# Optimization experiments

Measured on AMD Instinct MI355X. Metric: run time of the kernel, lower is better.

The kernel has to match this reference:

```python
import jax, jax.numpy as jnp
import numpy as np

TAU = 0.5
EPS = 1e-12  # torch F.normalize default eps


def setup_inputs() -> dict:
    key = jax.random.key(0)
    ks = jax.random.split(key, 6)
    N, D = 8192, 512
    return {
        "pri_embedding": jax.random.normal(ks[0], (N, D), dtype=jnp.float32),
        "aux_embedding": jax.random.normal(ks[1], (N, D), dtype=jnp.float32),
        "W1": jax.random.normal(ks[2], (D, D), dtype=jnp.float32) * (1.0 / np.sqrt(D)),
        "b1": jax.random.normal(ks[3], (D,), dtype=jnp.float32) * 0.01,
        "W2": jax.random.normal(ks[4], (D, D), dtype=jnp.float32) * (1.0 / np.sqrt(D)),
        "b2": jax.random.normal(ks[5], (D,), dtype=jnp.float32) * 0.01,
    }


def _projection(z, W1, b1, W2, b2):
    h = jax.nn.elu(z @ W1.T + b1)
    return h @ W2.T + b2


def _normalize(z):
    norm = jnp.sqrt(jnp.sum(z * z, axis=-1, keepdims=True))
    return z / jnp.maximum(norm, EPS)


def _semi_loss(z1, z2):
    n1 = _normalize(z1)
    n2 = _normalize(z2)
    refl = jnp.exp((n1 @ n1.T) / TAU)      # [N, N]
    between = jnp.exp((n1 @ n2.T) / TAU)   # [N, N]
    num = jnp.diagonal(between)
    den = refl.sum(axis=1) + between.sum(axis=1) - jnp.diagonal(refl)
    return -jnp.log(num / den)


def reference(pri_embedding, aux_embedding, W1, b1, W2, b2):
    h1 = _projection(pri_embedding, W1, b1, W2, b2)
    h2 = _projection(aux_embedding, W1, b1, W2, b2)
    l1 = _semi_loss(h1, h2)
    l2 = _semi_loss(h2, h1)
    ret = (l1 + l2) * 0.5
    return ret.mean()
```

## Files before the change

kernel.cpp:

```cpp
#include <hip/hip_runtime.h>
#include <stdint.h>

typedef unsigned short u16;
typedef __bf16 bf16x8 __attribute__((ext_vector_type(8)));
typedef float f32x4 __attribute__((ext_vector_type(4)));

#define NROWS 8192
#define DDIM 512

#define GLOAD_LDS16(g, l)                                            \
  __builtin_amdgcn_global_load_lds(                                  \
      (const __attribute__((address_space(1))) void*)(g),            \
      (__attribute__((address_space(3))) void*)(l), 16, 0, 0)

__device__ __forceinline__ u16 f32_to_bf16(float f) {
  union { float f; unsigned u; } v; v.f = f;
  unsigned r = v.u + 0x7fffu + ((v.u >> 16) & 1u);
  return (u16)(r >> 16);
}

#define GEMM_CORE(A_, B_)                                                     \
  const int t = threadIdx.x;                                                  \
  const int lane = t & 63;                                                    \
  const int w = t >> 6;                                                       \
  const int wr = w >> 1, wc = w & 1;                                          \
  const int r0 = t >> 2, c0 = (t & 3) * 8;                                    \
  const u16* ApA = A_ + (size_t)(tileM + r0) * 512 + c0;                      \
  const u16* ApB = ApA + (size_t)64 * 512;                                    \
  const u16* BpA = B_ + (size_t)(tileN + r0) * 512 + c0;                      \
  const u16* BpB = BpA + (size_t)64 * 512;                                    \
  f32x4 acc[4][4] = {};                                                       \
  const int lrow = lane & 15;                                                 \
  const int kb = (lane >> 4) * 8;                                             \
  for (int k0 = 0; k0 < 512; k0 += 64) {                                      \
    __syncthreads();                                                          \
    GLOAD_LDS16(ApA + k0,      &As[t * 8]);                                   \
    GLOAD_LDS16(ApB + k0,      &As[(t + 256) * 8]);                           \
    GLOAD_LDS16(ApA + k0 + 32, &As[(t + 512) * 8]);                           \
    GLOAD_LDS16(ApB + k0 + 32, &As[(t + 768) * 8]);                           \
    GLOAD_LDS16(BpA + k0,      &Bs[t * 8]);                                   \
    GLOAD_LDS16(BpB + k0,      &Bs[(t + 256) * 8]);                           \
    GLOAD_LDS16(BpA + k0 + 32, &Bs[(t + 512) * 8]);                           \
    GLOAD_LDS16(BpB + k0 + 32, &Bs[(t + 768) * 8]);                           \
    __syncthreads();                                                          \
    _Pragma("unroll")                                                         \
    for (int s = 0; s < 2; s++) {                                             \
      bf16x8 af[4], bfr[4];                                                   \
      _Pragma("unroll")                                                       \
      for (int m = 0; m < 4; m++)                                             \
        af[m] = *(const bf16x8*)&As[s * 4096 + (wr * 64 + m * 16 + lrow) * 32 + kb]; \
      _Pragma("unroll")                                                       \
      for (int n = 0; n < 4; n++)                                             \
        bfr[n] = *(const bf16x8*)&Bs[s * 4096 + (wc * 64 + n * 16 + lrow) * 32 + kb]; \
      _Pragma("unroll")                                                       \
      for (int m = 0; m < 4; m++)                                             \
        _Pragma("unroll")                                                     \
        for (int n = 0; n < 4; n++)                                           \
          acc[m][n] = __builtin_amdgcn_mfma_f32_16x16x32_bf16(af[m], bfr[n], acc[m][n], 0, 0, 0); \
    }                                                                         \
  }                                                                           \
  const int rowg = (lane >> 4) * 4;                                           \
  const int col = lane & 15;

__global__ void cast2_f32_bf16(const float* __restrict__ a, u16* __restrict__ oa, int n4a,
                               const float* __restrict__ b, u16* __restrict__ ob, int n4b) {
  int i = blockIdx.x * blockDim.x + threadIdx.x;
  const float* src; u16* dst;
  if (i < n4a) { src = a; dst = oa; }
  else if (i < n4a + n4b) { i -= n4a; src = b; dst = ob; }
  else return;
  float4 v = reinterpret_cast<const float4*>(src)[i];
  ushort4 o;
  o.x = f32_to_bf16(v.x); o.y = f32_to_bf16(v.y);
  o.z = f32_to_bf16(v.z); o.w = f32_to_bf16(v.w);
  reinterpret_cast<ushort4*>(dst)[i] = o;
}

template <int EPI>
__global__ void __launch_bounds__(256)
gemm_proj(const u16* __restrict__ Ag, const u16* __restrict__ Bg,
          const float* __restrict__ bias,
          u16* __restrict__ outB, float* __restrict__ outF)
{
  __shared__ __align__(16) u16 As[2 * 128 * 32];
  __shared__ __align__(16) u16 Bs[2 * 128 * 32];
  const int tileM = blockIdx.y * 128;
  const int tileN = blockIdx.x * 128;

  GEMM_CORE(Ag, Bg)

#pragma unroll
  for (int m = 0; m < 4; m++) {
    int grow = tileM + wr * 64 + m * 16 + rowg;
#pragma unroll
    for (int n = 0; n < 4; n++) {
      int gcol = tileN + wc * 64 + n * 16 + col;
      float bv = bias[gcol];
#pragma unroll
      for (int r = 0; r < 4; r++) {
        float v = acc[m][n][r] + bv;
        if (EPI == 0) {
          v = v > 0.0f ? v : (__expf(v) - 1.0f);
          outB[(size_t)(grow + r) * 512 + gcol] = f32_to_bf16(v);
        } else {
          outF[(size_t)(grow + r) * 512 + gcol] = v;
        }
      }
    }
  }
}

__global__ void __launch_bounds__(256)
sim_merged(const u16* __restrict__ n1, const u16* __restrict__ n2,
           float* __restrict__ rs11, float* __restrict__ rs12,
           float* __restrict__ cs12, float* __restrict__ rs22)
{
  __shared__ __align__(16) u16 As[2 * 128 * 32];
  __shared__ __align__(16) u16 Bs[2 * 128 * 32];

  int bid = blockIdx.x;
  const u16 *A, *B; float *rsum, *csum; bool sym; int by, bx;
  if (bid < 4096) {
    by = bid >> 6; bx = bid & 63;
    A = n1; B = n2; rsum = rs12; csum = cs12; sym = false;
  } else {
    int tau = bid - 4096;
    if (tau >= 2080) { tau -= 2080; A = n2; rsum = rs22; }
    else             {              A = n1; rsum = rs11; }
    B = A; csum = rsum; sym = true;
    by = (int)(64.5f - sqrtf(64.5f * 64.5f - 2.0f * (float)tau));
    if (by < 0) by = 0;
    while (64 * (by + 1) - ((by + 1) * by) / 2 <= tau) by++;
    while (64 * by - (by * (by - 1)) / 2 > tau) by--;
    bx = by + (tau - (64 * by - (by * (by - 1)) / 2));
  }
  const int tileM = by * 128, tileN = bx * 128;

  GEMM_CORE(A, B)

#pragma unroll
  for (int m = 0; m < 4; m++) {
#pragma unroll
    for (int r = 0; r < 4; r++) {
      float s = 0.0f;
#pragma unroll
      for (int n = 0; n < 4; n++) {
        float e = __expf(acc[m][n][r] * 2.0f);
        acc[m][n][r] = e;
        s += e;
      }
      s += __shfl_xor(s, 1);
      s += __shfl_xor(s, 2);
      s += __shfl_xor(s, 4);
      s += __shfl_xor(s, 8);
      if (col == 0)
        atomicAdd(&rsum[tileM + wr * 64 + m * 16 + rowg + r], s);
    }
  }
  if (!sym || tileM != tileN) {
    float* cdst = sym ? rsum : csum;
#pragma unroll
    for (int n = 0; n < 4; n++) {
      float s = 0.0f;
#pragma unroll
      for (int m = 0; m < 4; m++)
#pragma unroll
        for (int r = 0; r < 4; r++) s += acc[m][n][r];
      s += __shfl_xor(s, 16);
      s += __shfl_xor(s, 32);
      if ((lane >> 4) == 0)
        atomicAdd(&cdst[tileN + wc * 64 + n * 16 + col], s);
    }
  }
}

__global__ void __launch_bounds__(256)
normalize_rows(const float* __restrict__ p1, const float* __restrict__ p2,
               u16* __restrict__ n1, u16* __restrict__ n2, float* __restrict__ d12)
{
  int row = blockIdx.x;
  int t = threadIdx.x;
  const float* r1 = p1 + (size_t)row * 512;
  const float* r2 = p2 + (size_t)row * 512;
  float a0 = r1[t], a1 = r1[t + 256];
  float b0 = r2[t], b1 = r2[t + 256];
  float ss1 = a0 * a0 + a1 * a1;
  float ss2 = b0 * b0 + b1 * b1;
  float dt  = a0 * b0 + a1 * b1;
#pragma unroll
  for (int m = 1; m < 64; m <<= 1) {
    ss1 += __shfl_xor(ss1, m);
    ss2 += __shfl_xor(ss2, m);
    dt  += __shfl_xor(dt, m);
  }
  __shared__ float sh[3][4];
  int w = t >> 6;
  if ((t & 63) == 0) { sh[0][w] = ss1; sh[1][w] = ss2; sh[2][w] = dt; }
  __syncthreads();
  ss1 = sh[0][0] + sh[0][1] + sh[0][2] + sh[0][3];
  ss2 = sh[1][0] + sh[1][1] + sh[1][2] + sh[1][3];
  dt  = sh[2][0] + sh[2][1] + sh[2][2] + sh[2][3];
  float i1 = 1.0f / fmaxf(sqrtf(ss1), 1e-12f);
  float i2 = 1.0f / fmaxf(sqrtf(ss2), 1e-12f);
  n1[(size_t)row * 512 + t]       = f32_to_bf16(a0 * i1);
  n1[(size_t)row * 512 + t + 256] = f32_to_bf16(a1 * i1);
  n2[(size_t)row * 512 + t]       = f32_to_bf16(b0 * i2);
  n2[(size_t)row * 512 + t + 256] = f32_to_bf16(b1 * i2);
  if (t == 0) d12[row] = dt * i1 * i2;
}

__global__ void __launch_bounds__(256)
loss_reduce(const float* __restrict__ rs11, const float* __restrict__ rs12,
            const float* __restrict__ cs12, const float* __restrict__ rs22,
            const float* __restrict__ d12, float* __restrict__ out)
{
  int t = threadIdx.x;
  const float e2 = __expf(2.0f);
  float s = 0.0f;
  for (int i = t; i < NROWS; i += 256) {
    float den1 = rs11[i] + rs12[i] - e2;
    float den2 = rs22[i] + cs12[i] - e2;
    s += 0.5f * (logf(den1) + logf(den2)) - 2.0f * d12[i];
  }
#pragma unroll
  for (int m = 1; m < 64; m <<= 1) s += __shfl_xor(s, m);
  __shared__ float sh[4];
  if ((t & 63) == 0) sh[t >> 6] = s;
  __syncthreads();
  if (t == 0) out[0] = (sh[0] + sh[1] + sh[2] + sh[3]) * (1.0f / (float)NROWS);
}

extern "C" void kernel_launch(void* const* d_in, const int* in_sizes, int n_in,
                              void* d_out, int out_size, void* d_ws, size_t ws_size,
                              hipStream_t stream) {
  (void)in_sizes; (void)n_in; (void)out_size; (void)ws_size;
  const float* pri = (const float*)d_in[0];
  const float* aux = (const float*)d_in[1];
  const float* W1  = (const float*)d_in[2];
  const float* b1  = (const float*)d_in[3];
  const float* W2  = (const float*)d_in[4];
  const float* b2  = (const float*)d_in[5];
  float* out = (float*)d_out;

  const int N = NROWS, D = DDIM;
  char* ws = (char*)d_ws;
  size_t off = 0;
  auto alloc = [&](size_t bytes) -> void* {
    void* p = ws + off;
    off += (bytes + 255) & ~(size_t)255;
    return p;
  };
  u16* prib = (u16*)alloc((size_t)N * D * 2);
  u16* auxb = (u16*)alloc((size_t)N * D * 2);
  u16* W1b  = (u16*)alloc((size_t)D * D * 2);
  u16* W2b  = (u16*)alloc((size_t)D * D * 2);
  u16* h1b  = (u16*)alloc((size_t)N * D * 2);
  u16* h2b  = (u16*)alloc((size_t)N * D * 2);
  float* p1 = (float*)alloc((size_t)N * D * 4);
  float* p2 = (float*)alloc((size_t)N * D * 4);
  u16* n1b  = (u16*)alloc((size_t)N * D * 2);
  u16* n2b  = (u16*)alloc((size_t)N * D * 2);
  float* d12  = (float*)alloc((size_t)N * 4);
  float* rs11 = (float*)alloc((size_t)N * 4);
  float* rs12 = (float*)alloc((size_t)N * 4);
  float* cs12 = (float*)alloc((size_t)N * 4);
  float* rs22 = (float*)alloc((size_t)N * 4);
  (void)auxb; (void)h2b; (void)p2;

  hipMemsetAsync(rs11, 0, (size_t)4 * N * 4, stream);

  const int n4e = N * D / 4, n4w = D * D / 4;
  cast2_f32_bf16<<<(n4e + n4w + 255) / 256, 256, 0, stream>>>(pri, prib, n4e, W1, W1b, n4w);
  cast2_f32_bf16<<<(n4e + n4w + 255) / 256, 256, 0, stream>>>(aux, auxb, n4e, W2, W2b, n4w);

  dim3 gproj(D / 128, 2 * N / 128);
  gemm_proj<0><<<gproj, 256, 0, stream>>>(prib, W1b, b1, h1b, nullptr);
  gemm_proj<1><<<gproj, 256, 0, stream>>>(h1b, W2b, b2, nullptr, p1);

  normalize_rows<<<N, 256, 0, stream>>>(p1, p2, n1b, n2b, d12);

  sim_merged<<<4096 + 2 * 2080, 256, 0, stream>>>(n1b, n2b, rs11, rs12, cs12, rs22);

  loss_reduce<<<1, 256, 0, stream>>>(rs11, rs12, cs12, rs22, d12, out);
}
```

Before: 413.7 us.

## Enlarge similarity GEMM tiles to 256x256 with double-buffered LDS prefetch

The fused similarity/exp/row-sum kernel moves from 128x128 tiles with 256 threads to 256x256 tiles with 512 threads (8 waves, 128x64 per wave). The K loop now stages the next K-slice into a second LDS buffer while computing on the current one, so there is one barrier per step instead of two. Block indices are remapped so that consecutive launch IDs spread across groups of 260. The GEMM core macro is inlined into the projection kernel. The goal is more operand reuse per global/LDS load and fewer exposed memory stalls, at the cost of 128KB of LDS per block, which limits occupancy and coarsens work on the symmetric triangle.

```diff
diff --git a/kernel.cpp b/kernel.cpp
--- a/kernel.cpp
+++ b/kernel.cpp
@@ -18,49 +18,6 @@
   unsigned r = v.u + 0x7fffu + ((v.u >> 16) & 1u);
   return (u16)(r >> 16);
 }
-
-#define GEMM_CORE(A_, B_)                                                     \
-  const int t = threadIdx.x;                                                  \
-  const int lane = t & 63;                                                    \
-  const int w = t >> 6;                                                       \
-  const int wr = w >> 1, wc = w & 1;                                          \
-  const int r0 = t >> 2, c0 = (t & 3) * 8;                                    \
-  const u16* ApA = A_ + (size_t)(tileM + r0) * 512 + c0;                      \
-  const u16* ApB = ApA + (size_t)64 * 512;                                    \
-  const u16* BpA = B_ + (size_t)(tileN + r0) * 512 + c0;                      \
-  const u16* BpB = BpA + (size_t)64 * 512;                                    \
-  f32x4 acc[4][4] = {};                                                       \
-  const int lrow = lane & 15;                                                 \
-  const int kb = (lane >> 4) * 8;                                             \
-  for (int k0 = 0; k0 < 512; k0 += 64) {                                      \
-    __syncthreads();                                                          \
-    GLOAD_LDS16(ApA + k0,      &As[t * 8]);                                   \
-    GLOAD_LDS16(ApB + k0,      &As[(t + 256) * 8]);                           \
-    GLOAD_LDS16(ApA + k0 + 32, &As[(t + 512) * 8]);                           \
-    GLOAD_LDS16(ApB + k0 + 32, &As[(t + 768) * 8]);                           \
-    GLOAD_LDS16(BpA + k0,      &Bs[t * 8]);                                   \
-    GLOAD_LDS16(BpB + k0,      &Bs[(t + 256) * 8]);                           \
-    GLOAD_LDS16(BpA + k0 + 32, &Bs[(t + 512) * 8]);                           \
-    GLOAD_LDS16(BpB + k0 + 32, &Bs[(t + 768) * 8]);                           \
-    __syncthreads();                                                          \
-    _Pragma("unroll")                                                         \
-    for (int s = 0; s < 2; s++) {                                             \
-      bf16x8 af[4], bfr[4];                                                   \
-      _Pragma("unroll")                                                       \
-      for (int m = 0; m < 4; m++)                                             \
-        af[m] = *(const bf16x8*)&As[s * 4096 + (wr * 64 + m * 16 + lrow) * 32 + kb]; \
-      _Pragma("unroll")                                                       \
-      for (int n = 0; n < 4; n++)                                             \
-        bfr[n] = *(const bf16x8*)&Bs[s * 4096 + (wc * 64 + n * 16 + lrow) * 32 + kb]; \
-      _Pragma("unroll")                                                       \
-      for (int m = 0; m < 4; m++)                                             \
-        _Pragma("unroll")                                                     \
-        for (int n = 0; n < 4; n++)                                           \
-          acc[m][n] = __builtin_amdgcn_mfma_f32_16x16x32_bf16(af[m], bfr[n], acc[m][n], 0, 0, 0); \
-    }                                                                         \
-  }                                                                           \
-  const int rowg = (lane >> 4) * 4;                                           \
-  const int col = lane & 15;
 
 __global__ void cast2_f32_bf16(const float* __restrict__ a, u16* __restrict__ oa, int n4a,
                                const float* __restrict__ b, u16* __restrict__ ob, int n4b) {
@@ -87,8 +44,47 @@
   const int tileM = blockIdx.y * 128;
   const int tileN = blockIdx.x * 128;
 
-  GEMM_CORE(Ag, Bg)
-
+  const int t = threadIdx.x;
+  const int lane = t & 63;
+  const int w = t >> 6;
+  const int wr = w >> 1, wc = w & 1;
+  const int r0 = t >> 2, c0 = (t & 3) * 8;
+  const u16* ApA = Ag + (size_t)(tileM + r0) * 512 + c0;
+  const u16* ApB = ApA + (size_t)64 * 512;
+  const u16* BpA = Bg + (size_t)(tileN + r0) * 512 + c0;
+  const u16* BpB = BpA + (size_t)64 * 512;
+  f32x4 acc[4][4] = {};
+  const int lrow = lane & 15;
+  const int kb = (lane >> 4) * 8;
+  for (int k0 = 0; k0 < 512; k0 += 64) {
+    __syncthreads();
+    GLOAD_LDS16(ApA + k0,      &As[t * 8]);
+    GLOAD_LDS16(ApB + k0,      &As[(t + 256) * 8]);
+    GLOAD_LDS16(ApA + k0 + 32, &As[(t + 512) * 8]);
+    GLOAD_LDS16(ApB + k0 + 32, &As[(t + 768) * 8]);
+    GLOAD_LDS16(BpA + k0,      &Bs[t * 8]);
+    GLOAD_LDS16(BpB + k0,      &Bs[(t + 256) * 8]);
+    GLOAD_LDS16(BpA + k0 + 32, &Bs[(t + 512) * 8]);
+    GLOAD_LDS16(BpB + k0 + 32, &Bs[(t + 768) * 8]);
+    __syncthreads();
+#pragma unroll
+    for (int s = 0; s < 2; s++) {
+      bf16x8 af[4], bfr[4];
+#pragma unroll
+      for (int m = 0; m < 4; m++)
+        af[m] = *(const bf16x8*)&As[s * 4096 + (wr * 64 + m * 16 + lrow) * 32 + kb];
+#pragma unroll
+      for (int n = 0; n < 4; n++)
+        bfr[n] = *(const bf16x8*)&Bs[s * 4096 + (wc * 64 + n * 16 + lrow) * 32 + kb];
+#pragma unroll
+      for (int m = 0; m < 4; m++)
+#pragma unroll
+        for (int n = 0; n < 4; n++)
+          acc[m][n] = __builtin_amdgcn_mfma_f32_16x16x32_bf16(af[m], bfr[n], acc[m][n], 0, 0, 0);
+    }
+  }
+  const int rowg = (lane >> 4) * 4;
+  const int col = lane & 15;
 #pragma unroll
   for (int m = 0; m < 4; m++) {
     int grow = tileM + wr * 64 + m * 16 + rowg;
@@ -110,36 +106,94 @@
   }
 }
 
-__global__ void __launch_bounds__(256)
+__global__ void __launch_bounds__(512, 2)
 sim_merged(const u16* __restrict__ n1, const u16* __restrict__ n2,
            float* __restrict__ rs11, float* __restrict__ rs12,
            float* __restrict__ cs12, float* __restrict__ rs22)
 {
-  __shared__ __align__(16) u16 As[2 * 128 * 32];
-  __shared__ __align__(16) u16 Bs[2 * 128 * 32];
-
-  int bid = blockIdx.x;
+  __shared__ __align__(16) u16 AsF[2 * 2 * 256 * 32];
+  __shared__ __align__(16) u16 BsF[2 * 2 * 256 * 32];
+
+  int bid = (blockIdx.x & 7) * 260 + (blockIdx.x >> 3);
+
   const u16 *A, *B; float *rsum, *csum; bool sym; int by, bx;
-  if (bid < 4096) {
-    by = bid >> 6; bx = bid & 63;
+  if (bid < 1024) {
+    by = bid >> 5; bx = bid & 31;
     A = n1; B = n2; rsum = rs12; csum = cs12; sym = false;
   } else {
-    int tau = bid - 4096;
-    if (tau >= 2080) { tau -= 2080; A = n2; rsum = rs22; }
-    else             {              A = n1; rsum = rs11; }
+    int tau = bid - 1024;
+    if (tau >= 528) { tau -= 528; A = n2; rsum = rs22; }
+    else            {             A = n1; rsum = rs11; }
     B = A; csum = rsum; sym = true;
-    by = (int)(64.5f - sqrtf(64.5f * 64.5f - 2.0f * (float)tau));
+    by = (int)(32.5f - sqrtf(32.5f * 32.5f - 2.0f * (float)tau));
     if (by < 0) by = 0;
-    while (64 * (by + 1) - ((by + 1) * by) / 2 <= tau) by++;
-    while (64 * by - (by * (by - 1)) / 2 > tau) by--;
-    bx = by + (tau - (64 * by - (by * (by - 1)) / 2));
-  }
-  const int tileM = by * 128, tileN = bx * 128;
-
-  GEMM_CORE(A, B)
-
-#pragma unroll
-  for (int m = 0; m < 4; m++) {
+    while (32 * (by + 1) - ((by + 1) * by) / 2 <= tau) by++;
+    while (32 * by - (by * (by - 1)) / 2 > tau) by--;
+    bx = by + (tau - (32 * by - (by * (by - 1)) / 2));
+  }
+  const int tileM = by * 256, tileN = bx * 256;
+
+  const int t = threadIdx.x;
+  const int lane = t & 63;
+  const int w = t >> 6;
+  const int wr = w >> 2;
+  const int wc = w & 3;
+  const int lrow = lane & 15;
+  const int kb = (lane >> 4) * 8;
+
+  const u16* aP0 = A + (size_t)(tileM + (t >> 2)) * 512 + (t & 3) * 8;
+  const u16* bP0 = B + (size_t)(tileN + (t >> 2)) * 512 + (t & 3) * 8;
+
+#define STAGE_TILE(d, kt) {                                                   \
+    const int ko = (kt) * 64;                                                 \
+    GLOAD_LDS16(aP0 + ko,              &AsF[(d) * 16384 + t * 8]);            \
+    GLOAD_LDS16(aP0 + 65536 + ko,      &AsF[(d) * 16384 + 4096 + t * 8]);     \
+    GLOAD_LDS16(aP0 + ko + 32,         &AsF[(d) * 16384 + 8192 + t * 8]);     \
+    GLOAD_LDS16(aP0 + 65536 + ko + 32, &AsF[(d) * 16384 + 12288 + t * 8]);    \
+    GLOAD_LDS16(bP0 + ko,              &BsF[(d) * 16384 + t * 8]);            \
+    GLOAD_LDS16(bP0 + 65536 + ko,      &BsF[(d) * 16384 + 4096 + t * 8]);     \
+    GLOAD_LDS16(bP0 + ko + 32,         &BsF[(d) * 16384 + 8192 + t * 8]);     \
+    GLOAD_LDS16(bP0 + 65536 + ko + 32, &BsF[(d) * 16384 + 12288 + t * 8]);    \
+  }
+
+  f32x4 acc[8][4] = {};
+
+#define COMPUTE_TILE(d) {                                                     \
+    _Pragma("unroll")                                                         \
+    for (int s = 0; s < 2; s++) {                                             \
+      bf16x8 af[8], bfr[4];                                                   \
+      _Pragma("unroll")                                                       \
+      for (int m = 0; m < 8; m++)                                             \
+        af[m] = *(const bf16x8*)&AsF[(d) * 16384 + s * 8192 +                 \
+                                     (wr * 128 + m * 16 + lrow) * 32 + kb];   \
+      _Pragma("unroll")                                                       \
+      for (int n = 0; n < 4; n++)                                             \
+        bfr[n] = *(const bf16x8*)&BsF[(d) * 16384 + s * 8192 +                \
+                                      (wc * 64 + n * 16 + lrow) * 32 + kb];   \
+      _Pragma("unroll")                                                       \
+      for (int m = 0; m < 8; m++)                                             \
+        _Pragma("unroll")                                                     \
+        for (int n = 0; n < 4; n++)                                           \
+          acc[m][n] = __builtin_amdgcn_mfma_f32_16x16x32_bf16(af[m], bfr[n], acc[m][n], 0, 0, 0); \
+    }                                                                         \
+  }
+
+  STAGE_TILE(0, 0)
+  __syncthreads();
+  int cur = 0;
+  for (int kt = 0; kt < 7; ++kt) {
+    STAGE_TILE(cur ^ 1, kt + 1)
+    COMPUTE_TILE(cur)
+    __syncthreads();
+    cur ^= 1;
+  }
+  COMPUTE_TILE(cur)
+
+  const int rowg = (lane >> 4) * 4;
+  const int col = lane & 15;
+
+#pragma unroll
+  for (int m = 0; m < 8; m++) {
 #pragma unroll
     for (int r = 0; r < 4; r++) {
       float s = 0.0f;
@@ -154,7 +208,7 @@
       s += __shfl_xor(s, 4);
       s += __shfl_xor(s, 8);
       if (col == 0)
-        atomicAdd(&rsum[tileM + wr * 64 + m * 16 + rowg + r], s);
+        atomicAdd(&rsum[tileM + wr * 128 + m * 16 + rowg + r], s);
     }
   }
   if (!sym || tileM != tileN) {
@@ -163,7 +217,7 @@
     for (int n = 0; n < 4; n++) {
       float s = 0.0f;
 #pragma unroll
-      for (int m = 0; m < 4; m++)
+      for (int m = 0; m < 8; m++)
 #pragma unroll
         for (int r = 0; r < 4; r++) s += acc[m][n][r];
       s += __shfl_xor(s, 16);
@@ -172,6 +226,8 @@
         atomicAdd(&cdst[tileN + wc * 64 + n * 16 + col], s);
     }
   }
+#undef STAGE_TILE
+#undef COMPUTE_TILE
 }
 
 __global__ void __launch_bounds__(256)
@@ -279,7 +335,7 @@
 
   normalize_rows<<<N, 256, 0, stream>>>(p1, p2, n1b, n2b, d12);
 
-  sim_merged<<<4096 + 2 * 2080, 256, 0, stream>>>(n1b, n2b, rs11, rs12, cs12, rs22);
+  sim_merged<<<2080, 512, 0, stream>>>(n1b, n2b, rs11, rs12, cs12, rs22);
 
   loss_reduce<<<1, 256, 0, stream>>>(rs11, rs12, cs12, rs22, d12, out);
 }
```

Result: slower. 457.5 us (+10.6%).
